# Optimization experiments

Hardware: AMD Instinct MI355X
Metric: run time of the kernel (lower is better)

## Reference

```python
import jax, jax.numpy as jnp
import numpy as np

GRID_DIMS = (64, 64, 64)
GRID_LOWER = np.array([0.0, 0.0, 0.0], np.float32)
GRID_STEPS = np.array([0.015625, 0.015625, 0.015625], np.float32)
RADIUS = 0.03125
STENCIL = 2  # ceil(radius / step)


def _poly6(d2, h):
    # standard SPH poly6 smoothing kernel: 315/(64 pi h^9) (h^2 - d^2)^3, d <= h
    c = np.float32(315.0 / (64.0 * np.pi * h ** 9))
    return jnp.where(d2 <= h * h, c * (h * h - d2) ** 3, 0.0)


def particles2grid(locs, data, density):
    # locs [B,N,3], data [B,N,C], density [B,N] -> grid [B,X,Y,Z,C]
    B, N, _ = locs.shape
    C = data.shape[-1]
    X, Y, Z = GRID_DIMS
    dims = jnp.array(GRID_DIMS, jnp.int32)
    r = jnp.arange(-STENCIL, STENCIL + 1)
    offs = jnp.stack(jnp.meshgrid(r, r, r, indexing='ij'), -1).reshape(-1, 3)  # [K,3]
    base = jnp.floor((locs - GRID_LOWER) / GRID_STEPS).astype(jnp.int32)        # [B,N,3]
    cells = base[:, :, None, :] + offs                                          # [B,N,K,3]
    centers = GRID_LOWER + (cells.astype(locs.dtype) + 0.5) * GRID_STEPS
    d2 = jnp.sum((centers - locs[:, :, None, :]) ** 2, -1)                      # [B,N,K]
    w = _poly6(d2, RADIUS)
    w = jnp.where(jnp.all((cells >= 0) & (cells < dims), -1), w, 0.0)
    contrib = w[..., None] * (data / density[..., None])[:, :, None, :]         # [B,N,K,C]
    cells = jnp.clip(cells, 0, dims - 1)
    flat = (cells[..., 0] * Y + cells[..., 1]) * Z + cells[..., 2]              # [B,N,K]

    def splat(f, c):
        return jnp.zeros((X * Y * Z, C), data.dtype).at[f.reshape(-1)].add(c.reshape(-1, C))

    return jax.vmap(splat)(flat, contrib).reshape(B, X, Y, Z, C)


def grid2particles(grid, locs):
    # trilinear interpolation of grid [B,X,Y,Z,C] at particle locations [B,N,3]
    B, X, Y, Z, C = grid.shape
    dims = jnp.array([X, Y, Z], jnp.int32)
    pos = (locs - GRID_LOWER) / GRID_STEPS - 0.5                                # cell-center coords
    i0 = jnp.floor(pos).astype(jnp.int32)
    frac = pos - i0.astype(locs.dtype)
    gflat = grid.reshape(B, X * Y * Z, C)
    gather = jax.vmap(lambda g, f: g[f])                                        # [B,N] -> [B,N,C]
    out = jnp.zeros((B, locs.shape[1], C), grid.dtype)
    for dx in (0, 1):
        for dy in (0, 1):
            for dz in (0, 1):
                off = jnp.array([dx, dy, dz], jnp.int32)
                idx = i0 + off
                wd = jnp.where(off == 1, frac, 1.0 - frac)                      # [B,N,3]
                w = wd[..., 0] * wd[..., 1] * wd[..., 2]
                w = jnp.where(jnp.all((idx >= 0) & (idx < dims), -1), w, 0.0)
                idx = jnp.clip(idx, 0, dims - 1)
                flat = (idx[..., 0] * Y + idx[..., 1]) * Z + idx[..., 2]
                out = out + w[..., None] * gather(gflat, flat)
    return out


def conv3d(x, w, b):
    y = jax.lax.conv_general_dilated(x, w, (1, 1, 1), 'SAME',
                                     dimension_numbers=('NCDHW', 'OIDHW', 'NCDHW'))
    return y + b[None, :, None, None, None]


def prelu(x, a):
    return jnp.where(x >= 0, x, a * x)


def setup_inputs() -> dict:
    key = jax.random.key(0)
    ks = jax.random.split(key, 8)
    B, N = 2, 32768
    Cin, K, Cout = 4, 32, 4
    s = lambda fan: np.float32(1.0 / np.sqrt(fan * 27))
    return {
        'locs': jax.random.uniform(ks[0], (B, N, 3), jnp.float32),
        'data': jax.random.normal(ks[1], (B, N, Cin), jnp.float32),
        'density': jax.random.uniform(ks[2], (B, N), jnp.float32, 0.5, 1.5),
        'W0': jax.random.normal(ks[3], (K, Cin, 3, 3, 3), jnp.float32) * s(Cin),
        'b0': jnp.zeros((K,), jnp.float32),
        'W1': jax.random.normal(ks[4], (K, K, 3, 3, 3), jnp.float32) * s(K),
        'b1': jnp.zeros((K,), jnp.float32),
        'W2': jax.random.normal(ks[5], (K, K, 3, 3, 3), jnp.float32) * s(K),
        'b2': jnp.zeros((K,), jnp.float32),
        'W3': jax.random.normal(ks[6], (Cout, K, 3, 3, 3), jnp.float32) * s(K),
        'b3': jnp.zeros((Cout,), jnp.float32),
        'a0': jnp.full((1,), 0.25, jnp.float32),
        'a1': jnp.full((1,), 0.25, jnp.float32),
        'a2': jnp.full((1,), 0.25, jnp.float32),
    }


def reference(locs, data, density, W0, b0, W1, b1, W2, b2, W3, b3, a0, a1, a2):
    grid = particles2grid(locs, data, density)            # [B,X,Y,Z,Cin]
    g = jnp.transpose(grid, (0, 4, 1, 2, 3))              # NCDHW
    g = prelu(conv3d(g, W0, b0), a0)
    g = prelu(conv3d(g, W1, b1), a1)
    g = prelu(conv3d(g, W2, b2), a2)
    g = conv3d(g, W3, b3)
    g = jnp.transpose(g, (0, 2, 3, 4, 1))                 # [B,X,Y,Z,Cout]
    return grid2particles(g, locs)                        # [B,N,Cout]
```

## Files before the change

kernel.cpp:

```cpp
#include <hip/hip_runtime.h>

#define BATCH 2
#define NPART 32768
#define GD 64
#define NVOX (BATCH * GD * GD * GD)

typedef unsigned short ushortT;
typedef __attribute__((ext_vector_type(8))) short short8;
typedef __attribute__((ext_vector_type(16))) float float16;

__device__ __forceinline__ float poly6_c() {
    const double H9 = 1.0 / 35184372088832.0;
    return (float)(315.0 / (64.0 * 3.14159265358979323846 * H9));
}

__device__ __forceinline__ ushortT bf16_rne(float f) {
    unsigned int u = __float_as_uint(f);
    u = (u + 0x7fffu + ((u >> 16) & 1u)) >> 16;
    return (ushortT)u;
}

__device__ __forceinline__ int imax(int a, int b) { return a > b ? a : b; }
__device__ __forceinline__ int imin(int a, int b) { return a < b ? a : b; }

__device__ __forceinline__ void load_lds16(const void* g, void* l) {
    __builtin_amdgcn_global_load_lds(
        (const __attribute__((address_space(1))) void*)g,
        (__attribute__((address_space(3))) void*)l, 16, 0, 0);
}

__global__ void zero_ints_kernel(int* __restrict__ p, int n) {
    int t = blockIdx.x * blockDim.x + threadIdx.x;
    if (t < n) p[t] = 0;
}

__global__ __launch_bounds__(256) void bin_count_kernel(
    const float* __restrict__ locs, int* __restrict__ counts) {
    int t = blockIdx.x * blockDim.x + threadIdx.x;
    if (t >= BATCH * NPART) return;
    int b = t >> 15;
    int bx = ((int)floorf(locs[t * 3 + 0] * 64.0f)) >> 1;
    int by = ((int)floorf(locs[t * 3 + 1] * 64.0f)) >> 1;
    int bz = ((int)floorf(locs[t * 3 + 2] * 64.0f)) >> 1;
    atomicAdd(&counts[b * 32768 + ((bx * 32) + by) * 32 + bz], 1);
}

__global__ __launch_bounds__(256) void scanA_kernel(
    const int* __restrict__ counts, int* __restrict__ offsets,
    int* __restrict__ blockSum) {
    __shared__ int sh[256];
    int tid = threadIdx.x, g = blockIdx.x;
    int v = counts[g * 256 + tid];
    sh[tid] = v;
    __syncthreads();
    for (int off = 1; off < 256; off <<= 1) {
        int u = (tid >= off) ? sh[tid - off] : 0;
        __syncthreads();
        sh[tid] += u;
        __syncthreads();
    }
    offsets[g * 256 + tid] = sh[tid] - v;
    if (tid == 255) blockSum[g] = sh[255];
}

__global__ __launch_bounds__(256) void scanB_kernel(
    int* __restrict__ offsets, const int* __restrict__ blockSum) {
    __shared__ int sh[256];
    int tid = threadIdx.x, g = blockIdx.x;
    sh[tid] = (tid < g) ? blockSum[tid] : 0;
    __syncthreads();
    for (int off = 128; off > 0; off >>= 1) {
        if (tid < off) sh[tid] += sh[tid + off];
        __syncthreads();
    }
    offsets[g * 256 + tid] += sh[0];
    if (g == 255 && tid == 255) offsets[65536] = BATCH * NPART;
}

__global__ __launch_bounds__(256) void bin_scatter_kernel(
    const float* __restrict__ locs, const float* __restrict__ data,
    const float* __restrict__ density, const int* __restrict__ offsets,
    int* __restrict__ cursor, float* __restrict__ payload) {
    int t = blockIdx.x * blockDim.x + threadIdx.x;
    if (t >= BATCH * NPART) return;
    int b = t >> 15;
    float px = locs[t * 3 + 0];
    float py = locs[t * 3 + 1];
    float pz = locs[t * 3 + 2];
    int bx = ((int)floorf(px * 64.0f)) >> 1;
    int by = ((int)floorf(py * 64.0f)) >> 1;
    int bz = ((int)floorf(pz * 64.0f)) >> 1;
    int bb = b * 32768 + ((bx * 32) + by) * 32 + bz;
    int slot = atomicAdd(&cursor[bb], 1);
    int idx = offsets[bb] + slot;
    float inv_d = 1.0f / density[t];
    float4 p0 = {px, py, pz, data[t * 4 + 0] * inv_d};
    float4 p1 = {data[t * 4 + 1] * inv_d, data[t * 4 + 2] * inv_d,
                 data[t * 4 + 3] * inv_d, 0.f};
    *(float4*)(payload + idx * 8)     = p0;
    *(float4*)(payload + idx * 8 + 4) = p1;
}

__global__ __launch_bounds__(256) void splat_gather_kernel(
    const float* __restrict__ payload, const int* __restrict__ offsets,
    ushortT* __restrict__ g8) {
    __shared__ float plist[256 * 8];
    __shared__ int segS[36];
    __shared__ int segP[37];
    __shared__ int shTot[1];

    int wg = blockIdx.x;
    int sb = wg & 511, b = wg >> 9;
    int X0 = (sb >> 6) * 8, Y0 = ((sb >> 3) & 7) * 8, Z0 = (sb & 7) * 8;
    int tid = threadIdx.x;

    int bxlo = imax(0, (X0 - 2) >> 1), bxhi = imin(31, (X0 + 9) >> 1);
    int bylo = imax(0, (Y0 - 2) >> 1), byhi = imin(31, (Y0 + 9) >> 1);
    int bzlo = imax(0, (Z0 - 2) >> 1), bzhi = imin(31, (Z0 + 9) >> 1);
    int ny = byhi - bylo + 1;
    int ns = (bxhi - bxlo + 1) * ny;
    if (tid < ns) {
        int bx = bxlo + tid / ny, by = bylo + tid % ny;
        int row = b * 32768 + (bx * 32 + by) * 32;
        int s = offsets[row + bzlo];
        int e = offsets[row + bzhi + 1];
        segS[tid] = s;
        segP[tid] = e - s;
    }
    __syncthreads();
    if (tid == 0) {
        int p = 0;
        for (int k = 0; k < ns; ++k) { int len = segP[k]; segP[k] = p; p += len; }
        segP[ns] = p;
        shTot[0] = p;
    }
    __syncthreads();

    const float step = 0.015625f;
    const float h2 = 0.03125f * 0.03125f;
    const float cc = poly6_c();
    int total = shTot[0];

    int l = tid & 63, w = tid >> 6;
    int cx = X0 + 4 * (w >> 1) + (l >> 4);
    int cy = Y0 + 4 * (w & 1) + ((l >> 2) & 3);
    int cz0 = Z0 + (l & 3);
    float xc  = ((float)cx  + 0.5f) * step;
    float yc  = ((float)cy  + 0.5f) * step;
    float zc0 = ((float)cz0 + 0.5f) * step;
    float zc1 = zc0 + 4.0f * step;

    float a00 = 0.f, a01 = 0.f, a02 = 0.f, a03 = 0.f;
    float a10 = 0.f, a11 = 0.f, a12 = 0.f, a13 = 0.f;

    int nchunks = (total + 255) >> 8;
    for (int ch = 0; ch < nchunks; ++ch) {
        __syncthreads();
        int jj = (ch << 8) + tid;
        if (jj < total) {
            int k = 0;
            while (jj >= segP[k + 1]) ++k;
            int idx = segS[k] + (jj - segP[k]);
            *(float4*)(plist + tid * 8)     = *(const float4*)(payload + idx * 8);
            *(float4*)(plist + tid * 8 + 4) = *(const float4*)(payload + idx * 8 + 4);
        }
        __syncthreads();
        int cnt = imin(256, total - (ch << 8));
        for (int p = 0; p < cnt; ++p) {
            float4 pa = *(const float4*)(plist + p * 8);
            float dx = pa.x - xc, dy = pa.y - yc;
            float dxy2 = fmaf(dy, dy, dx * dx);
            if (!__any(dxy2 <= h2)) continue;
            float4 pv = *(const float4*)(plist + p * 8 + 4);
            float dz0 = pa.z - zc0;
            float d20 = fmaf(dz0, dz0, dxy2);
            float u0 = fmaxf(h2 - d20, 0.f);
            float w0 = (cc * u0) * (u0 * u0);
            a00 = fmaf(w0, pa.w, a00);
            a01 = fmaf(w0, pv.x, a01);
            a02 = fmaf(w0, pv.y, a02);
            a03 = fmaf(w0, pv.z, a03);
            float dz1 = pa.z - zc1;
            float d21 = fmaf(dz1, dz1, dxy2);
            float u1 = fmaxf(h2 - d21, 0.f);
            float w1 = (cc * u1) * (u1 * u1);
            a10 = fmaf(w1, pa.w, a10);
            a11 = fmaf(w1, pv.x, a11);
            a12 = fmaf(w1, pv.y, a12);
            a13 = fmaf(w1, pv.z, a13);
        }
    }

    size_t cellBase = (size_t)(((b * 64 + cx) * 64 + cy) * 64);
    short8 o;
    o[0] = (short)bf16_rne(a00); o[1] = (short)bf16_rne(a01);
    o[2] = (short)bf16_rne(a02); o[3] = (short)bf16_rne(a03);
    o[4] = 0; o[5] = 0; o[6] = 0; o[7] = 0;
    *(short8*)(g8 + (cellBase + cz0) * 8) = o;
    o[0] = (short)bf16_rne(a10); o[1] = (short)bf16_rne(a11);
    o[2] = (short)bf16_rne(a12); o[3] = (short)bf16_rne(a13);
    *(short8*)(g8 + (cellBase + cz0 + 4) * 8) = o;
}

__global__ void repack_all_kernel(
    const float* __restrict__ W0, const float* __restrict__ W1,
    const float* __restrict__ W2, const float* __restrict__ W3,
    short* __restrict__ Bp) {
    int t = blockIdx.x * blockDim.x + threadIdx.x;
    if (t >= 176 * 512) return;
    int kt = t >> 9;
    int l = (t >> 3) & 63, j = t & 7;
    int n = l & 31, q = l >> 5;
    float v = 0.f;
    if (kt < 14) {
        int k = kt * 16 + 8 * q + j;
        int tap = k / 8, ic = k - tap * 8;
        if (tap < 27 && ic < 4) v = W0[(n * 4 + ic) * 27 + tap];
    } else {
        int rem = kt - 14;
        const float* W; int O;
        if (rem < 54)       { W = W1; O = 32; }
        else if (rem < 108) { W = W2; O = 32; rem -= 54; }
        else                { W = W3; O = 4;  rem -= 108; }
        int p = rem / 27, tap = rem - p * 27;
        int ic = p * 16 + q * 8 + j;
        if (n < O) v = W[(n * 32 + ic) * 27 + tap];
    }
    Bp[t] = (short)bf16_rne(v);
}

template <int ICG, int KT, bool FINAL>
__global__ __launch_bounds__(256) void mfma_conv_kernel(
    const ushortT* __restrict__ in, const short* __restrict__ Bpack,
    const float* __restrict__ bias, const float* __restrict__ alpha,
    const float* __restrict__ zguard, void* __restrict__ outv) {
    constexpr int CIN = ICG * 8;
    constexpr int NPH  = (ICG == 4) ? 2 : 1;
    constexpr int ICGH = (ICG == 4) ? 2 : 1;
    constexpr int NCHH = 24 * ICGH * 34;
    constexpr int KTH  = KT / NPH;
    __shared__ short lds[NCHH * 8];
    int wg = ((blockIdx.x & 7) << 8) | (blockIdx.x >> 3);
    int zh = wg & 1, yq = (wg >> 1) & 15, xp = (wg >> 5) & 31, b = wg >> 10;
    int X0 = xp * 2, Y0 = yq * 4, Z0 = zh * 32;
    int tid = threadIdx.x;

    const ushortT* inb = in + (size_t)b * (64 * 64 * 64 * CIN);

    int l = tid & 63, w = tid >> 6;
    int wx = w >> 1;
    int cyA = (w & 1) * 2, cyB = cyA + 1;
    int n = l & 31, q = l >> 5;

    float bval = FINAL ? (n < 4 ? bias[n] : 0.f) : bias[n];
    float16 accA, accB;
#pragma unroll
    for (int r = 0; r < 16; ++r) { accA[r] = bval; accB[r] = bval; }

    const short* bp = Bpack + (size_t)l * 8;
    int laneZ = (l & 31) * 8;

#pragma unroll
    for (int p = 0; p < NPH; ++p) {
        if (p) __syncthreads();
#pragma unroll
        for (int it = 0; it < (NCHH + 255) / 256; ++it) {
            int ccid = it * 256 + tid;
            if (ccid < NCHH) {
                int col  = ccid / (ICGH * 34);
                int rem  = ccid - col * (ICGH * 34);
                int icgL = rem / 34;
                int zi   = rem - icgL * 34;
                int gx = X0 + col / 6 - 1;
                int gy = Y0 + col % 6 - 1;
                int gz = Z0 + zi - 1;
                const void* src = (const void*)zguard;
                if ((unsigned)gx < 64u && (unsigned)gy < 64u && (unsigned)gz < 64u)
                    src = (const void*)(inb + ((size_t)(((gx * 64) + gy) * 64 + gz)) * CIN
                                        + (p * ICGH + icgL) * 8);
                load_lds16(src, (void*)(lds + ccid * 8));
            }
        }
        __syncthreads();

        const short* bph = bp + (size_t)(p * KTH) * 512;
        short8 bf[4];
#pragma unroll
        for (int i = 0; i < 4; ++i) bf[i] = *(const short8*)(bph + i * 512);

#pragma unroll
        for (int t = 0; t < KTH; ++t) {
            short8 bcur = bf[t & 3];
            if (t + 4 < KTH) bf[t & 3] = *(const short8*)(bph + (t + 4) * 512);
            int aofsA, aofsB;
            if constexpr (ICG == 1) {
                int tap0 = t * 2, tap1 = t * 2 + 1;
                if (tap1 > 26) tap1 = 26;
                int dx0 = tap0 / 9, r0 = tap0 - dx0 * 9, dy0 = r0 / 3, dz0 = r0 - dy0 * 3;
                int dx1 = tap1 / 9, r1 = tap1 - dx1 * 9, dy1 = r1 / 3, dz1 = r1 - dy1 * 3;
                int cA0 = (((wx + dx0) * 6 + (cyA + dy0)) * 34 + dz0) * 8;
                int cA1 = (((wx + dx1) * 6 + (cyA + dy1)) * 34 + dz1) * 8;
                int cB0 = (((wx + dx0) * 6 + (cyB + dy0)) * 34 + dz0) * 8;
                int cB1 = (((wx + dx1) * 6 + (cyB + dy1)) * 34 + dz1) * 8;
                aofsA = q ? cA1 : cA0;
                aofsB = q ? cB1 : cB0;
            } else {
                int dx = t / 9, rr = t - dx * 9, dy = rr / 3, dz = rr - dy * 3;
                aofsA = ((((wx + dx) * 6 + (cyA + dy)) * 2 + q) * 34 + dz) * 8;
                aofsB = ((((wx + dx) * 6 + (cyB + dy)) * 2 + q) * 34 + dz) * 8;
            }
            short8 afragA = *(const short8*)(lds + aofsA + laneZ);
            short8 afragB = *(const short8*)(lds + aofsB + laneZ);
            accA = __builtin_amdgcn_mfma_f32_32x32x16_bf16(afragA, bcur, accA, 0, 0, 0);
            accB = __builtin_amdgcn_mfma_f32_32x32x16_bf16(afragB, bcur, accB, 0, 0, 0);
        }
    }

    size_t baseA = (size_t)(((b * 64 + X0 + wx) * 64 + (Y0 + cyA)) * 64) + Z0;
    size_t baseB = (size_t)(((b * 64 + X0 + wx) * 64 + (Y0 + cyB)) * 64) + Z0;
    if (FINAL) {
        float* out = (float*)outv;
        if (n < 4) {
#pragma unroll
            for (int r = 0; r < 16; ++r) {
                int z = (r & 3) + 8 * (r >> 2) + 4 * q;
                out[(baseA + z) * 4 + n] = accA[r];
                out[(baseB + z) * 4 + n] = accB[r];
            }
        }
    } else {
        float a = alpha[0];
        ushortT* out = (ushortT*)outv;
#pragma unroll
        for (int r = 0; r < 16; ++r) {
            int z = (r & 3) + 8 * (r >> 2) + 4 * q;
            float vA = accA[r];
            vA = vA >= 0.f ? vA : a * vA;
            out[(baseA + z) * 32 + n] = bf16_rne(vA);
            float vB = accB[r];
            vB = vB >= 0.f ? vB : a * vB;
            out[(baseB + z) * 32 + n] = bf16_rne(vB);
        }
    }
}

__global__ __launch_bounds__(256) void gather_kernel(
    const float* __restrict__ grid, const float* __restrict__ locs,
    float* __restrict__ out) {
    int t = blockIdx.x * blockDim.x + threadIdx.x;
    if (t >= BATCH * NPART) return;
    int b = t >> 15;

    float px = locs[t * 3 + 0] * 64.0f - 0.5f;
    float py = locs[t * 3 + 1] * 64.0f - 0.5f;
    float pz = locs[t * 3 + 2] * 64.0f - 0.5f;
    int ix = (int)floorf(px);
    int iy = (int)floorf(py);
    int iz = (int)floorf(pz);
    float fx = px - (float)ix;
    float fy = py - (float)iy;
    float fz = pz - (float)iz;

    const float* gb = grid + (size_t)b * GD * GD * GD * 4;
    float o0 = 0.f, o1 = 0.f, o2 = 0.f, o3 = 0.f;

#pragma unroll
    for (int dx = 0; dx < 2; ++dx) {
        int x = ix + dx;
        if ((unsigned)x > 63u) continue;
        float wx = dx ? fx : 1.0f - fx;
#pragma unroll
        for (int dy = 0; dy < 2; ++dy) {
            int y = iy + dy;
            if ((unsigned)y > 63u) continue;
            float wy = dy ? fy : 1.0f - fy;
#pragma unroll
            for (int dz = 0; dz < 2; ++dz) {
                int z = iz + dz;
                if ((unsigned)z > 63u) continue;
                float wz = dz ? fz : 1.0f - fz;
                float w = wx * wy * wz;
                const float4 g = *(const float4*)(gb + (size_t)(((x * GD) + y) * GD + z) * 4);
                o0 += w * g.x; o1 += w * g.y; o2 += w * g.z; o3 += w * g.w;
            }
        }
    }
    out[t * 4 + 0] = o0;
    out[t * 4 + 1] = o1;
    out[t * 4 + 2] = o2;
    out[t * 4 + 3] = o3;
}

extern "C" void kernel_launch(void* const* d_in, const int* in_sizes, int n_in,
                              void* d_out, int out_size, void* d_ws, size_t ws_size,
                              hipStream_t stream) {
    const float* locs    = (const float*)d_in[0];
    const float* data    = (const float*)d_in[1];
    const float* density = (const float*)d_in[2];
    const float* W0 = (const float*)d_in[3];
    const float* b0 = (const float*)d_in[4];
    const float* W1 = (const float*)d_in[5];
    const float* b1 = (const float*)d_in[6];
    const float* W2 = (const float*)d_in[7];
    const float* b2 = (const float*)d_in[8];
    const float* W3 = (const float*)d_in[9];
    const float* b3 = (const float*)d_in[10];
    const float* a0 = (const float*)d_in[11];
    const float* a1 = (const float*)d_in[12];
    const float* a2 = (const float*)d_in[13];
    float* out = (float*)d_out;

    char* ws = (char*)d_ws;
    ushortT* g8  = (ushortT*)(ws);
    ushortT* gA  = (ushortT*)(ws + 8388608);
    ushortT* gB  = (ushortT*)(ws + 41943040);
    float*  gF   = (float*)(ws + 75497472);
    short*  Bp   = (short*)(ws + 83886080);
    short*  Bp0  = Bp;
    short*  Bp1  = Bp + 14 * 512;
    short*  Bp2  = Bp + 68 * 512;
    short*  Bp3  = Bp + 122 * 512;
    float* zguard   = (float*)(ws + 84066240);
    int*   counts   = (int*)(ws + 84066304);
    int*   cursor   = (int*)(ws + 84328448);
    int*   offsets  = (int*)(ws + 84590592);
    int*   blockSum = (int*)(ws + 84852752);
    float* payload  = (float*)(ws + 84853888);

    zero_ints_kernel<<<(131088 + 255) / 256, 256, 0, stream>>>((int*)zguard, 131088);
    bin_count_kernel<<<(BATCH * NPART) / 256, 256, 0, stream>>>(locs, counts);
    scanA_kernel<<<256, 256, 0, stream>>>(counts, offsets, blockSum);
    scanB_kernel<<<256, 256, 0, stream>>>(offsets, blockSum);
    bin_scatter_kernel<<<(BATCH * NPART) / 256, 256, 0, stream>>>(
        locs, data, density, offsets, cursor, payload);

    repack_all_kernel<<<(176 * 512 + 255) / 256, 256, 0, stream>>>(W0, W1, W2, W3, Bp);

    splat_gather_kernel<<<BATCH * 512, 256, 0, stream>>>(payload, offsets, g8);

    const int CGRID = 2048;
    mfma_conv_kernel< 1, 14, false><<<CGRID, 256, 0, stream>>>(g8, Bp0, b0, a0, zguard, gA);
    mfma_conv_kernel< 4, 54, false><<<CGRID, 256, 0, stream>>>(gA, Bp1, b1, a1, zguard, gB);
    mfma_conv_kernel< 4, 54, false><<<CGRID, 256, 0, stream>>>(gB, Bp2, b2, a2, zguard, gA);
    mfma_conv_kernel< 4, 54, true ><<<CGRID, 256, 0, stream>>>(gA, Bp3, b3, b3, zguard, gF);

    gather_kernel<<<(BATCH * NPART) / 256, 256, 0, stream>>>(gF, locs, out);
}
```

Measured before the change: 255.4 us.

## Drop LDS staging in conv; read padded channel-group-major grids directly from global

```diff
diff --git a/kernel.cpp b/kernel.cpp
--- a/kernel.cpp
+++ b/kernel.cpp
@@ -23,15 +23,23 @@
 __device__ __forceinline__ int imax(int a, int b) { return a > b ? a : b; }
 __device__ __forceinline__ int imin(int a, int b) { return a < b ? a : b; }
 
-__device__ __forceinline__ void load_lds16(const void* g, void* l) {
-    __builtin_amdgcn_global_load_lds(
-        (const __attribute__((address_space(1))) void*)g,
-        (__attribute__((address_space(3))) void*)l, 16, 0, 0);
-}
-
 __global__ void zero_ints_kernel(int* __restrict__ p, int n) {
     int t = blockIdx.x * blockDim.x + threadIdx.x;
     if (t < n) p[t] = 0;
+}
+
+__global__ void zero_borders_kernel(ushortT* __restrict__ g8,
+                                    ushortT* __restrict__ gA,
+                                    ushortT* __restrict__ gB) {
+    int t = blockIdx.x * 256 + threadIdx.x;
+    if (t >= 147456) return;
+    ushortT* base; int idx;
+    if (t < 16384)      { base = g8; idx = t; }
+    else if (t < 81920) { base = gA; idx = t - 16384; }
+    else                { base = gB; idx = t - 81920; }
+    int slot = (idx & 1) * 65; idx >>= 1;
+    short8 z8 = {0, 0, 0, 0, 0, 0, 0, 0};
+    *(short8*)(base + ((size_t)idx * 66 + slot) * 8) = z8;
 }
 
 __global__ __launch_bounds__(256) void bin_count_kernel(
@@ -191,15 +199,15 @@
         }
     }
 
-    size_t cellBase = (size_t)(((b * 64 + cx) * 64 + cy) * 64);
+    size_t colIdx = (size_t)(((b * 64 + cx) * 64) + cy);
     short8 o;
     o[0] = (short)bf16_rne(a00); o[1] = (short)bf16_rne(a01);
     o[2] = (short)bf16_rne(a02); o[3] = (short)bf16_rne(a03);
     o[4] = 0; o[5] = 0; o[6] = 0; o[7] = 0;
-    *(short8*)(g8 + (cellBase + cz0) * 8) = o;
+    *(short8*)(g8 + (colIdx * 66 + (cz0 + 1)) * 8) = o;
     o[0] = (short)bf16_rne(a10); o[1] = (short)bf16_rne(a11);
     o[2] = (short)bf16_rne(a12); o[3] = (short)bf16_rne(a13);
-    *(short8*)(g8 + (cellBase + cz0 + 4) * 8) = o;
+    *(short8*)(g8 + (colIdx * 66 + (cz0 + 5)) * 8) = o;
 }
 
 __global__ void repack_all_kernel(
@@ -233,24 +241,22 @@
 __global__ __launch_bounds__(256) void mfma_conv_kernel(
     const ushortT* __restrict__ in, const short* __restrict__ Bpack,
     const float* __restrict__ bias, const float* __restrict__ alpha,
-    const float* __restrict__ zguard, void* __restrict__ outv) {
-    constexpr int CIN = ICG * 8;
-    constexpr int NPH  = (ICG == 4) ? 2 : 1;
-    constexpr int ICGH = (ICG == 4) ? 2 : 1;
-    constexpr int NCHH = 24 * ICGH * 34;
-    constexpr int KTH  = KT / NPH;
-    __shared__ short lds[NCHH * 8];
+    const ushortT* __restrict__ zg, void* __restrict__ outv) {
+    constexpr int CST = ICG * 528;
     int wg = ((blockIdx.x & 7) << 8) | (blockIdx.x >> 3);
     int zh = wg & 1, yq = (wg >> 1) & 15, xp = (wg >> 5) & 31, b = wg >> 10;
     int X0 = xp * 2, Y0 = yq * 4, Z0 = zh * 32;
     int tid = threadIdx.x;
-
-    const ushortT* inb = in + (size_t)b * (64 * 64 * 64 * CIN);
-
     int l = tid & 63, w = tid >> 6;
-    int wx = w >> 1;
-    int cyA = (w & 1) * 2, cyB = cyA + 1;
+    int wx = w >> 1, cyl = (w & 1) * 2;
     int n = l & 31, q = l >> 5;
+
+    const ushortT* inb = in + (size_t)b * 4096 * CST;
+    int Xc = X0 + wx - 1;
+    int YcA = Y0 + cyl - 1;
+    const ushortT* cornA = inb + (ptrdiff_t)(Xc * 64 + YcA) * CST;
+    const ushortT* cornB = cornA + CST;
+    int laneOff = (Z0 + (l & 31)) * 8 + ((ICG == 4) ? q * 528 : 0);
 
     float bval = FINAL ? (n < 4 ? bias[n] : 0.f) : bias[n];
     float16 accA, accB;
@@ -258,68 +264,65 @@
     for (int r = 0; r < 16; ++r) { accA[r] = bval; accB[r] = bval; }
 
     const short* bp = Bpack + (size_t)l * 8;
-    int laneZ = (l & 31) * 8;
-
-#pragma unroll
-    for (int p = 0; p < NPH; ++p) {
-        if (p) __syncthreads();
-#pragma unroll
-        for (int it = 0; it < (NCHH + 255) / 256; ++it) {
-            int ccid = it * 256 + tid;
-            if (ccid < NCHH) {
-                int col  = ccid / (ICGH * 34);
-                int rem  = ccid - col * (ICGH * 34);
-                int icgL = rem / 34;
-                int zi   = rem - icgL * 34;
-                int gx = X0 + col / 6 - 1;
-                int gy = Y0 + col % 6 - 1;
-                int gz = Z0 + zi - 1;
-                const void* src = (const void*)zguard;
-                if ((unsigned)gx < 64u && (unsigned)gy < 64u && (unsigned)gz < 64u)
-                    src = (const void*)(inb + ((size_t)(((gx * 64) + gy) * 64 + gz)) * CIN
-                                        + (p * ICGH + icgL) * 8);
-                load_lds16(src, (void*)(lds + ccid * 8));
-            }
-        }
-        __syncthreads();
-
-        const short* bph = bp + (size_t)(p * KTH) * 512;
-        short8 bf[4];
-#pragma unroll
-        for (int i = 0; i < 4; ++i) bf[i] = *(const short8*)(bph + i * 512);
-
-#pragma unroll
-        for (int t = 0; t < KTH; ++t) {
-            short8 bcur = bf[t & 3];
-            if (t + 4 < KTH) bf[t & 3] = *(const short8*)(bph + (t + 4) * 512);
-            int aofsA, aofsB;
-            if constexpr (ICG == 1) {
-                int tap0 = t * 2, tap1 = t * 2 + 1;
-                if (tap1 > 26) tap1 = 26;
-                int dx0 = tap0 / 9, r0 = tap0 - dx0 * 9, dy0 = r0 / 3, dz0 = r0 - dy0 * 3;
-                int dx1 = tap1 / 9, r1 = tap1 - dx1 * 9, dy1 = r1 / 3, dz1 = r1 - dy1 * 3;
-                int cA0 = (((wx + dx0) * 6 + (cyA + dy0)) * 34 + dz0) * 8;
-                int cA1 = (((wx + dx1) * 6 + (cyA + dy1)) * 34 + dz1) * 8;
-                int cB0 = (((wx + dx0) * 6 + (cyB + dy0)) * 34 + dz0) * 8;
-                int cB1 = (((wx + dx1) * 6 + (cyB + dy1)) * 34 + dz1) * 8;
-                aofsA = q ? cA1 : cA0;
-                aofsB = q ? cB1 : cB0;
-            } else {
-                int dx = t / 9, rr = t - dx * 9, dy = rr / 3, dz = rr - dy * 3;
-                aofsA = ((((wx + dx) * 6 + (cyA + dy)) * 2 + q) * 34 + dz) * 8;
-                aofsB = ((((wx + dx) * 6 + (cyB + dy)) * 2 + q) * 34 + dz) * 8;
-            }
-            short8 afragA = *(const short8*)(lds + aofsA + laneZ);
-            short8 afragB = *(const short8*)(lds + aofsB + laneZ);
-            accA = __builtin_amdgcn_mfma_f32_32x32x16_bf16(afragA, bcur, accA, 0, 0, 0);
-            accB = __builtin_amdgcn_mfma_f32_32x32x16_bf16(afragB, bcur, accB, 0, 0, 0);
-        }
-    }
-
-    size_t baseA = (size_t)(((b * 64 + X0 + wx) * 64 + (Y0 + cyA)) * 64) + Z0;
-    size_t baseB = (size_t)(((b * 64 + X0 + wx) * 64 + (Y0 + cyB)) * 64) + Z0;
+
+    auto loadAB = [&](int kt, short8& aA, short8& aB) {
+        if constexpr (ICG == 4) {
+            int p = kt / 27, t = kt - p * 27;
+            int dx = t / 9, rr = t - dx * 9, dy = rr / 3, dz = rr - dy * 3;
+            int K = (dx * 64 + dy) * CST + p * 1056 + dz * 8;
+            bool xv = (unsigned)(Xc + dx) < 64u;
+            bool vA = xv && (unsigned)(YcA + dy) < 64u;
+            bool vB = xv && (unsigned)(YcA + 1 + dy) < 64u;
+            const ushortT* bA = vA ? cornA + K : zg;
+            const ushortT* bB = vB ? cornB + K : zg;
+            aA = *(const short8*)(bA + laneOff);
+            aB = *(const short8*)(bB + laneOff);
+        } else {
+            int t0 = kt * 2;
+            int t1 = (kt * 2 + 1 > 26) ? 26 : kt * 2 + 1;
+            int dx0 = t0 / 9, r0 = t0 - dx0 * 9, dy0 = r0 / 3, dz0 = r0 - dy0 * 3;
+            int dx1 = t1 / 9, r1 = t1 - dx1 * 9, dy1 = r1 / 3, dz1 = r1 - dy1 * 3;
+            int K0 = (dx0 * 64 + dy0) * CST + dz0 * 8;
+            int K1 = (dx1 * 64 + dy1) * CST + dz1 * 8;
+            bool v0A = (unsigned)(Xc + dx0) < 64u && (unsigned)(YcA + dy0) < 64u;
+            bool v1A = (unsigned)(Xc + dx1) < 64u && (unsigned)(YcA + dy1) < 64u;
+            bool v0B = (unsigned)(Xc + dx0) < 64u && (unsigned)(YcA + 1 + dy0) < 64u;
+            bool v1B = (unsigned)(Xc + dx1) < 64u && (unsigned)(YcA + 1 + dy1) < 64u;
+            const ushortT* a0 = v0A ? cornA + K0 : zg;
+            const ushortT* a1 = v1A ? cornA + K1 : zg;
+            const ushortT* b0 = v0B ? cornB + K0 : zg;
+            const ushortT* b1 = v1B ? cornB + K1 : zg;
+            const ushortT* sA = q ? a1 : a0;
+            const ushortT* sB = q ? b1 : b0;
+            aA = *(const short8*)(sA + laneOff);
+            aB = *(const short8*)(sB + laneOff);
+        }
+    };
+
+    short8 bf[4], fA[4], fB[4];
+#pragma unroll
+    for (int i = 0; i < 4; ++i) {
+        bf[i] = *(const short8*)(bp + i * 512);
+        loadAB(i, fA[i], fB[i]);
+    }
+
+#pragma unroll
+    for (int kt = 0; kt < KT; ++kt) {
+        short8 bcur = bf[kt & 3];
+        short8 aA = fA[kt & 3];
+        short8 aB = fB[kt & 3];
+        if (kt + 4 < KT) {
+            bf[kt & 3] = *(const short8*)(bp + (kt + 4) * 512);
+            loadAB(kt + 4, fA[kt & 3], fB[kt & 3]);
+        }
+        accA = __builtin_amdgcn_mfma_f32_32x32x16_bf16(aA, bcur, accA, 0, 0, 0);
+        accB = __builtin_amdgcn_mfma_f32_32x32x16_bf16(aB, bcur, accB, 0, 0, 0);
+    }
+
     if (FINAL) {
         float* out = (float*)outv;
+        size_t baseA = (size_t)(((b * 64 + X0 + wx) * 64 + (Y0 + cyl)) * 64) + Z0;
+        size_t baseB = baseA + 64;
         if (n < 4) {
 #pragma unroll
             for (int r = 0; r < 16; ++r) {
@@ -331,15 +334,19 @@
     } else {
         float a = alpha[0];
         ushortT* out = (ushortT*)outv;
+        size_t colA = (size_t)((b * 64 + X0 + wx) * 64 + (Y0 + cyl));
+        ushortT* oA = out + colA * 2112 + (size_t)(n >> 3) * 528 + (n & 7);
+        ushortT* oB = oA + 2112;
 #pragma unroll
         for (int r = 0; r < 16; ++r) {
             int z = (r & 3) + 8 * (r >> 2) + 4 * q;
+            int zs = (Z0 + z + 1) * 8;
             float vA = accA[r];
             vA = vA >= 0.f ? vA : a * vA;
-            out[(baseA + z) * 32 + n] = bf16_rne(vA);
+            oA[zs] = bf16_rne(vA);
             float vB = accB[r];
             vB = vB >= 0.f ? vB : a * vB;
-            out[(baseB + z) * 32 + n] = bf16_rne(vB);
+            oB[zs] = bf16_rne(vB);
         }
     }
 }
@@ -412,22 +419,23 @@
 
     char* ws = (char*)d_ws;
     ushortT* g8  = (ushortT*)(ws);
-    ushortT* gA  = (ushortT*)(ws + 8388608);
-    ushortT* gB  = (ushortT*)(ws + 41943040);
-    float*  gF   = (float*)(ws + 75497472);
-    short*  Bp   = (short*)(ws + 83886080);
+    ushortT* gA  = (ushortT*)(ws + 8650752);
+    ushortT* gB  = (ushortT*)(ws + 43253760);
+    float*  gF   = (float*)(ws + 77856768);
+    short*  Bp   = (short*)(ws + 86245376);
     short*  Bp0  = Bp;
     short*  Bp1  = Bp + 14 * 512;
     short*  Bp2  = Bp + 68 * 512;
     short*  Bp3  = Bp + 122 * 512;
-    float* zguard   = (float*)(ws + 84066240);
-    int*   counts   = (int*)(ws + 84066304);
-    int*   cursor   = (int*)(ws + 84328448);
-    int*   offsets  = (int*)(ws + 84590592);
-    int*   blockSum = (int*)(ws + 84852752);
-    float* payload  = (float*)(ws + 84853888);
-
-    zero_ints_kernel<<<(131088 + 255) / 256, 256, 0, stream>>>((int*)zguard, 131088);
+    ushortT* zguard = (ushortT*)(ws + 86425600);
+    int*   counts   = (int*)(ws + 86429824);
+    int*   cursor   = (int*)(ws + 86691968);
+    int*   offsets  = (int*)(ws + 86954112);
+    int*   blockSum = (int*)(ws + 87216384);
+    float* payload  = (float*)(ws + 87217408);
+
+    zero_ints_kernel<<<(132128 + 255) / 256, 256, 0, stream>>>((int*)zguard, 132128);
+    zero_borders_kernel<<<576, 256, 0, stream>>>(g8, gA, gB);
     bin_count_kernel<<<(BATCH * NPART) / 256, 256, 0, stream>>>(locs, counts);
     scanA_kernel<<<256, 256, 0, stream>>>(counts, offsets, blockSum);
     scanB_kernel<<<256, 256, 0, stream>>>(offsets, blockSum);
```

Measured after the change: 269.1 us. +5.3%, slower.
